# Performance work log

Measured on AMD Instinct MI355X. Metric: run time of the kernel, lower is better.

Reference implementation:

```python
import jax, jax.numpy as jnp
import numpy as np

B, S, D = 4, 2048, 1024
E, K, H = 8, 2, 4096


def setup_inputs() -> dict:
    key = jax.random.key(0)
    ks = jax.random.split(key, 8)
    sd = 1.0 / np.sqrt(D)
    sh = 1.0 / np.sqrt(H)
    x = jax.random.normal(ks[0], (B, S, D), dtype=jnp.float32)
    gate_w = jax.random.normal(ks[1], (D, E), dtype=jnp.float32) * sd
    gate_b = jnp.zeros((E,), dtype=jnp.float32)
    w1 = jax.random.normal(ks[2], (E, D, H), dtype=jnp.float32) * sd
    b1 = jnp.zeros((E, H), dtype=jnp.float32)
    w2 = jax.random.normal(ks[3], (E, H, D), dtype=jnp.float32) * sh
    b2 = jnp.zeros((E, D), dtype=jnp.float32)
    return {"x": x, "gate_w": gate_w, "gate_b": gate_b,
            "w1": w1, "b1": b1, "w2": w2, "b2": b2}


def reference(x, gate_w, gate_b, w1, b1, w2, b2):
    # gate logits [B,S,E]
    logits = jnp.einsum('bsd,de->bse', x, gate_w) + gate_b
    # top-k over experts, softmax over the k selected (dim=2), in float32
    weights, selected = jax.lax.top_k(logits, K)            # [B,S,K]
    weights = jax.nn.softmax(weights.astype(jnp.float32), axis=-1).astype(x.dtype)
    out = jnp.zeros_like(x)
    for i in range(E):
        # per-token combine weight for expert i (0 if not routed here)
        w_i = jnp.sum(jnp.where(selected == i, weights, 0.0), axis=-1)  # [B,S]
        h = jax.nn.gelu(jnp.einsum('bsd,dh->bsh', x, w1[i]) + b1[i])    # [B,S,H]
        y = jnp.einsum('bsh,hd->bsd', h, w2[i]) + b2[i]                  # [B,S,D]
        out = out + w_i[..., None] * y
    return out
```

## Files before the change

kernel.cpp:

```cpp
#include <hip/hip_runtime.h>
#include <hip/hip_bf16.h>
#include <stdint.h>

#define T_TOK 8192
#define D_DIM 1024
#define E_NUM 8
#define H_DIM 4096
#define WL_MAX 72

typedef short bf16x8 __attribute__((ext_vector_type(8)));
typedef float f32x4 __attribute__((ext_vector_type(4)));

#define AS1 __attribute__((address_space(1)))
#define AS3 __attribute__((address_space(3)))

__device__ __forceinline__ unsigned short f2b(float f) {
  union { float f; uint32_t u; } v; v.f = f;
  uint32_t r = (v.u + 0x7fffu + ((v.u >> 16) & 1u)) >> 16;
  return (unsigned short)r;
}

__device__ __forceinline__ float gelu_tanh(float x) {
  float u = 0.7978845608028654f * (x + 0.044715f * x * x * x);
  u = fminf(fmaxf(u, -15.f), 15.f);
  float e = __expf(2.f * u);
  float t = (e - 1.f) / (e + 1.f);
  return 0.5f * x * (1.f + t);
}

__device__ __forceinline__ void gload_lds16(const void* g, void* l) {
  __builtin_amdgcn_global_load_lds((const AS1 uint32_t*)g, (AS3 uint32_t*)l, 16, 0, 0);
}

__global__ __launch_bounds__(256) void moe_gate_conv(const float* __restrict__ x,
                                                     const float* __restrict__ gw,
                                                     const float* __restrict__ gb,
                                                     unsigned short* __restrict__ xb,
                                                     int2* __restrict__ sel,
                                                     float2* __restrict__ wts,
                                                     int* __restrict__ meta) {
  int lane = threadIdx.x & 63;
  int t = blockIdx.x * 4 + (threadIdx.x >> 6);
  const float* xr = x + (size_t)t * D_DIM;
  unsigned short* xo = xb + (size_t)t * D_DIM;
  float acc[8];
#pragma unroll
  for (int e = 0; e < 8; e++) acc[e] = 0.f;
#pragma unroll
  for (int i = 0; i < 4; i++) {
    int d0 = lane * 4 + i * 256;
    float4 xv = *(const float4*)(xr + d0);
    ushort4 o;
    o.x = f2b(xv.x); o.y = f2b(xv.y); o.z = f2b(xv.z); o.w = f2b(xv.w);
    *(ushort4*)(xo + d0) = o;
    const float* gp = gw + (size_t)d0 * 8;
    float xs[4] = {xv.x, xv.y, xv.z, xv.w};
#pragma unroll
    for (int j = 0; j < 4; j++) {
#pragma unroll
      for (int e = 0; e < 8; e++) acc[e] += xs[j] * gp[j * 8 + e];
    }
  }
#pragma unroll
  for (int off = 32; off > 0; off >>= 1) {
#pragma unroll
    for (int e = 0; e < 8; e++) acc[e] += __shfl_xor(acc[e], off);
  }
  if (lane == 0) {
    float lg[8];
#pragma unroll
    for (int e = 0; e < 8; e++) lg[e] = acc[e] + gb[e];
    int e0 = 0; float b0 = lg[0];
#pragma unroll
    for (int e = 1; e < 8; e++) if (lg[e] > b0) { b0 = lg[e]; e0 = e; }
    int e1 = -1; float b1v = -1e30f;
#pragma unroll
    for (int e = 0; e < 8; e++) if (e != e0 && lg[e] > b1v) { b1v = lg[e]; e1 = e; }
    float d = __expf(b1v - b0);
    float w0 = 1.f / (1.f + d), w1 = d / (1.f + d);
    sel[t] = make_int2(e0, e1);
    wts[t] = make_float2(w0, w1);
    atomicAdd(&meta[e0], 1);
    atomicAdd(&meta[e1], 1);
  }
}

__global__ __launch_bounds__(256) void moe_transpose(const float* __restrict__ in,
                                                     unsigned short* __restrict__ out,
                                                     int R, int C) {
  int e = blockIdx.z;
  int c0 = blockIdx.x * 64, r0 = blockIdx.y * 64;
  __shared__ float tile[64][65];
  const float* ine = in + (size_t)e * R * C;
  unsigned short* oute = out + (size_t)e * R * C;
  int tr = threadIdx.x >> 2;
  int tc4 = (threadIdx.x & 3) * 16;
#pragma unroll
  for (int p = 0; p < 4; p++) {
    int c = tc4 + p * 4;
    float4 v = *(const float4*)(ine + (size_t)(r0 + tr) * C + c0 + c);
    tile[tr][c] = v.x; tile[tr][c + 1] = v.y; tile[tr][c + 2] = v.z; tile[tr][c + 3] = v.w;
  }
  __syncthreads();
#pragma unroll
  for (int p = 0; p < 4; p++) {
    int rr = tc4 + p * 4;
    ushort4 o;
    o.x = f2b(tile[rr + 0][tr]);
    o.y = f2b(tile[rr + 1][tr]);
    o.z = f2b(tile[rr + 2][tr]);
    o.w = f2b(tile[rr + 3][tr]);
    *(ushort4*)(oute + (size_t)(c0 + tr) * R + r0 + rr) = o;
  }
}

__global__ void moe_scan(int* meta, int2* wl) {
  if (threadIdx.x == 0 && blockIdx.x == 0) {
    int o = 0;
    for (int e = 0; e < 8; e++) { meta[8 + e] = o; meta[20 + e] = o; o += meta[e]; }
    meta[16] = o;
    int w = 0;
    for (int e = 0; e < 8; e++)
      for (int m0 = 0; m0 < meta[e]; m0 += 256) wl[w++] = make_int2(e, m0);
    meta[17] = w;
  }
}

__global__ __launch_bounds__(256) void moe_scatter(const int2* __restrict__ sel,
                                                   const float2* __restrict__ wts,
                                                   int* __restrict__ meta,
                                                   int* __restrict__ token_id,
                                                   float* __restrict__ weightv) {
  int t = blockIdx.x * 256 + threadIdx.x;
  if (t >= T_TOK) return;
  int2 s = sel[t];
  float2 w = wts[t];
  int p0 = atomicAdd(&meta[20 + s.x], 1); token_id[p0] = t; weightv[p0] = w.x;
  int p1 = atomicAdd(&meta[20 + s.y], 1); token_id[p1] = t; weightv[p1] = w.y;
}

__global__ __launch_bounds__(256) void moe_outinit(const int2* __restrict__ sel,
                                                   const float2* __restrict__ wts,
                                                   const float* __restrict__ b2,
                                                   float* __restrict__ out) {
  int t = blockIdx.x;
  int d = threadIdx.x * 4;
  int2 s = sel[t];
  float2 w = wts[t];
  float4 a = *(const float4*)(b2 + (size_t)s.x * D_DIM + d);
  float4 b = *(const float4*)(b2 + (size_t)s.y * D_DIM + d);
  float4 o;
  o.x = w.x * a.x + w.y * b.x;
  o.y = w.x * a.y + w.y * b.y;
  o.z = w.x * a.z + w.y * b.z;
  o.w = w.x * a.w + w.y * b.w;
  *(float4*)(out + (size_t)t * D_DIM + d) = o;
}

template<int MODE>
__global__ __launch_bounds__(512, 2) void moe_gemm_pipe(
    const unsigned short* __restrict__ Amat,
    const unsigned short* __restrict__ Bmat,
    const float* __restrict__ bias,
    const int* __restrict__ meta,
    const int2* __restrict__ wl,
    const int* __restrict__ token_id,
    const float* __restrict__ weightv,
    unsigned short* __restrict__ hout,
    float* __restrict__ yout) {
  constexpr int KLEN = MODE ? 4096 : 1024;
  constexpr int NK   = MODE ? 64 : 32;

  int wi = blockIdx.y;
  if (wi >= meta[17]) return;
  int e = wl[wi].x, m0 = wl[wi].y;
  int seg = meta[8 + e], ne = meta[9 + e] - seg;
  int n0, kbase;
  if (MODE) { n0 = (int)(blockIdx.x >> 1) * 256; kbase = (int)(blockIdx.x & 1) * 2048; }
  else      { n0 = blockIdx.x * 256; kbase = 0; }

  __shared__ unsigned short As[3][8192];
  __shared__ unsigned short Bs[3][8192];

  int tid = threadIdx.x, lane = tid & 63, w = tid >> 6;
  int wm = w >> 2, wn = w & 3;

  int binv = (lane & 0x38) | ((lane ^ (lane >> 2)) & 6) | ((lane ^ (lane >> 2) ^ (lane >> 4)) & 1);

  const unsigned short* aSrc[2];
  const unsigned short* bSrc[2];
#pragma unroll
  for (int q = 0; q < 2; ++q) {
    int lchunk = ((w * 2 + q) << 6) | binv;
    int row = lchunk >> 2;
    int ko = (lchunk & 3) * 8;
    int gi = m0 + row; if (gi >= ne) gi = m0;
    if (MODE) aSrc[q] = Amat + (size_t)(seg + gi) * KLEN + kbase + ko;
    else      aSrc[q] = Amat + (size_t)token_id[seg + gi] * KLEN + ko;
    bSrc[q] = Bmat + (size_t)e * (4096 * 1024) + (size_t)(n0 + row) * KLEN + kbase + ko;
  }

  auto STAGE = [&](int buf, int kt) {
#pragma unroll
    for (int q = 0; q < 2; ++q) {
      gload_lds16(aSrc[q] + kt * 32, &As[buf][(w * 2 + q) * 512]);
      gload_lds16(bSrc[q] + kt * 32, &Bs[buf][(w * 2 + q) * 512]);
    }
  };

  f32x4 acc[8][4] = {};
  const int aoff = (((wm * 128 + (lane & 15)) * 32 + (lane >> 4) * 8)) ^ ((lane & 7) << 3);
  const int boff = (((wn * 64 + (lane & 15)) * 32 + (lane >> 4) * 8)) ^ ((lane & 7) << 3);

  STAGE(0, 0); STAGE(1, 1);

  int cur = 0, sb = 2;
  for (int t = 0; t < NK; ++t) {
    if (t + 1 < NK) { asm volatile("s_waitcnt vmcnt(4)" ::: "memory"); }
    else            { asm volatile("s_waitcnt vmcnt(0)" ::: "memory"); }
    __builtin_amdgcn_s_barrier();
    if (t + 2 < NK) STAGE(sb, t + 2);
    bf16x8 af[8], bv8[4];
#pragma unroll
    for (int mf = 0; mf < 8; ++mf) af[mf] = *(const bf16x8*)&As[cur][aoff + mf * 512];
#pragma unroll
    for (int nf = 0; nf < 4; ++nf) bv8[nf] = *(const bf16x8*)&Bs[cur][boff + nf * 512];
    __builtin_amdgcn_s_setprio(1);
#pragma unroll
    for (int mf = 0; mf < 8; ++mf)
#pragma unroll
      for (int nf = 0; nf < 4; ++nf)
        acc[mf][nf] = __builtin_amdgcn_mfma_f32_16x16x32_bf16(af[mf], bv8[nf], acc[mf][nf], 0, 0, 0);
    __builtin_amdgcn_s_setprio(0);
    __builtin_amdgcn_sched_barrier(0);
    cur = (cur == 2) ? 0 : cur + 1;
    sb  = (sb  == 2) ? 0 : sb  + 1;
  }

  int rb = wm * 128 + (lane >> 4) * 4;
  int cb = n0 + wn * 64 + (lane & 15);
  if (MODE) {
#pragma unroll
    for (int mf = 0; mf < 8; ++mf) {
#pragma unroll
      for (int j = 0; j < 4; ++j) {
        int gi = m0 + rb + mf * 16 + j;
        if (gi < ne) {
          int p = seg + gi;
          int tok = token_id[p];
          float wt = weightv[p];
          float* orow = yout + (size_t)tok * D_DIM + cb;
#pragma unroll
          for (int nf = 0; nf < 4; ++nf)
            atomicAdd(&orow[nf * 16], wt * acc[mf][nf][j]);
        }
      }
    }
  } else {
    const float* be = bias + (size_t)e * H_DIM + cb;
    float bvv[4];
#pragma unroll
    for (int nf = 0; nf < 4; ++nf) bvv[nf] = be[nf * 16];
#pragma unroll
    for (int mf = 0; mf < 8; ++mf) {
#pragma unroll
      for (int j = 0; j < 4; ++j) {
        int gi = m0 + rb + mf * 16 + j;
        if (gi < ne) {
          unsigned short* hrow = hout + (size_t)(seg + gi) * H_DIM + cb;
#pragma unroll
          for (int nf = 0; nf < 4; ++nf)
            hrow[nf * 16] = f2b(gelu_tanh(acc[mf][nf][j] + bvv[nf]));
        }
      }
    }
  }
}

extern "C" void kernel_launch(void* const* d_in, const int* in_sizes, int n_in,
                              void* d_out, int out_size, void* d_ws, size_t ws_size,
                              hipStream_t stream) {
  const float* x      = (const float*)d_in[0];
  const float* gate_w = (const float*)d_in[1];
  const float* gate_b = (const float*)d_in[2];
  const float* w1     = (const float*)d_in[3];
  const float* b1     = (const float*)d_in[4];
  const float* w2     = (const float*)d_in[5];
  const float* b2     = (const float*)d_in[6];
  float* out = (float*)d_out;

  uint8_t* ws = (uint8_t*)d_ws;
  unsigned short* hbuf = (unsigned short*)(ws);
  unsigned short* xb   = (unsigned short*)(ws + 134217728ull);
  unsigned short* w1t  = (unsigned short*)(ws + 150994944ull);
  unsigned short* w2t  = (unsigned short*)(ws + 218103808ull);
  int*    token_id = (int*)  (ws + 285212672ull);
  float*  weightv  = (float*)(ws + 285278208ull);
  float2* wts      = (float2*)(ws + 285343744ull);
  int2*   sel      = (int2*) (ws + 285409280ull);
  int*    meta     = (int*)  (ws + 285474816ull);
  int2*   wl       = (int2*) (ws + 285475328ull);

  hipMemsetAsync(meta, 0, 512, stream);

  moe_gate_conv<<<dim3(T_TOK / 4), 256, 0, stream>>>(x, gate_w, gate_b, xb, sel, wts, meta);
  moe_transpose<<<dim3(H_DIM / 64, D_DIM / 64, E_NUM), 256, 0, stream>>>(w1, w1t, D_DIM, H_DIM);
  moe_transpose<<<dim3(D_DIM / 64, H_DIM / 64, E_NUM), 256, 0, stream>>>(w2, w2t, H_DIM, D_DIM);
  moe_scan<<<1, 64, 0, stream>>>(meta, wl);
  moe_scatter<<<dim3(T_TOK / 256), 256, 0, stream>>>(sel, wts, meta, token_id, weightv);
  moe_outinit<<<dim3(T_TOK), 256, 0, stream>>>(sel, wts, b2, out);

  moe_gemm_pipe<0><<<dim3(H_DIM / 256, WL_MAX), 512, 0, stream>>>(
      xb, w1t, b1, meta, wl, token_id, weightv, hbuf, nullptr);

  moe_gemm_pipe<1><<<dim3((D_DIM / 256) * 2, WL_MAX), 512, 0, stream>>>(
      hbuf, w2t, nullptr, meta, wl, token_id, weightv, nullptr, out);
}
```

Before: 971.7 us.

## Restructure MoE GEMM to 4-stage pipeline with split A/B staging and expert-interleaved grid

After: 975.0 us. No clear change (+0.3%).

```diff
diff --git a/kernel.cpp b/kernel.cpp
--- a/kernel.cpp
+++ b/kernel.cpp
@@ -6,7 +6,7 @@
 #define D_DIM 1024
 #define E_NUM 8
 #define H_DIM 4096
-#define WL_MAX 72
+#define PPX 10
 
 typedef short bf16x8 __attribute__((ext_vector_type(8)));
 typedef float f32x4 __attribute__((ext_vector_type(4)));
@@ -114,15 +114,11 @@
   }
 }
 
-__global__ void moe_scan(int* meta, int2* wl) {
+__global__ void moe_scan(int* meta) {
   if (threadIdx.x == 0 && blockIdx.x == 0) {
     int o = 0;
     for (int e = 0; e < 8; e++) { meta[8 + e] = o; meta[20 + e] = o; o += meta[e]; }
     meta[16] = o;
-    int w = 0;
-    for (int e = 0; e < 8; e++)
-      for (int m0 = 0; m0 < meta[e]; m0 += 256) wl[w++] = make_int2(e, m0);
-    meta[17] = w;
   }
 }
 
@@ -158,12 +154,11 @@
 }
 
 template<int MODE>
-__global__ __launch_bounds__(512, 2) void moe_gemm_pipe(
+__global__ __launch_bounds__(512, 2) void moe_gemm8p(
     const unsigned short* __restrict__ Amat,
     const unsigned short* __restrict__ Bmat,
     const float* __restrict__ bias,
     const int* __restrict__ meta,
-    const int2* __restrict__ wl,
     const int* __restrict__ token_id,
     const float* __restrict__ weightv,
     unsigned short* __restrict__ hout,
@@ -171,70 +166,99 @@
   constexpr int KLEN = MODE ? 4096 : 1024;
   constexpr int NK   = MODE ? 64 : 32;
 
-  int wi = blockIdx.y;
-  if (wi >= meta[17]) return;
-  int e = wl[wi].x, m0 = wl[wi].y;
+  int b = blockIdx.x;
+  int e = b & 7;
+  int u = b >> 3;
+  int n0, ps, kbase;
+  if (MODE) { n0 = (u & 3) * 256; kbase = ((u >> 2) & 1) * 2048; ps = u >> 3; }
+  else      { n0 = (u & 15) * 256; kbase = 0; ps = u >> 4; }
   int seg = meta[8 + e], ne = meta[9 + e] - seg;
-  int n0, kbase;
-  if (MODE) { n0 = (int)(blockIdx.x >> 1) * 256; kbase = (int)(blockIdx.x & 1) * 2048; }
-  else      { n0 = blockIdx.x * 256; kbase = 0; }
-
-  __shared__ unsigned short As[3][8192];
-  __shared__ unsigned short Bs[3][8192];
+  int m0 = ps * 256;
+  if (m0 >= ne) return;
+
+  __shared__ unsigned short As[4][8192];
+  __shared__ unsigned short Bs[4][8192];
 
   int tid = threadIdx.x, lane = tid & 63, w = tid >> 6;
   int wm = w >> 2, wn = w & 3;
 
-  int binv = (lane & 0x38) | ((lane ^ (lane >> 2)) & 6) | ((lane ^ (lane >> 2) ^ (lane >> 4)) & 1);
-
+  int srow = tid >> 2;
+  int sko  = (tid & 3) * 8;
   const unsigned short* aSrc[2];
   const unsigned short* bSrc[2];
 #pragma unroll
-  for (int q = 0; q < 2; ++q) {
-    int lchunk = ((w * 2 + q) << 6) | binv;
-    int row = lchunk >> 2;
-    int ko = (lchunk & 3) * 8;
-    int gi = m0 + row; if (gi >= ne) gi = m0;
-    if (MODE) aSrc[q] = Amat + (size_t)(seg + gi) * KLEN + kbase + ko;
-    else      aSrc[q] = Amat + (size_t)token_id[seg + gi] * KLEN + ko;
-    bSrc[q] = Bmat + (size_t)e * (4096 * 1024) + (size_t)(n0 + row) * KLEN + kbase + ko;
-  }
-
-  auto STAGE = [&](int buf, int kt) {
-#pragma unroll
-    for (int q = 0; q < 2; ++q) {
-      gload_lds16(aSrc[q] + kt * 32, &As[buf][(w * 2 + q) * 512]);
-      gload_lds16(bSrc[q] + kt * 32, &Bs[buf][(w * 2 + q) * 512]);
-    }
+  for (int h = 0; h < 2; ++h) {
+    int gi = m0 + h * 128 + srow; if (gi >= ne) gi = m0;
+    if (MODE) aSrc[h] = Amat + (size_t)(seg + gi) * KLEN + kbase + sko;
+    else      aSrc[h] = Amat + (size_t)token_id[seg + gi] * KLEN + sko;
+    bSrc[h] = Bmat + (size_t)e * (4096 * 1024)
+                   + (size_t)(n0 + h * 128 + srow) * KLEN + kbase + sko;
+  }
+
+  auto stageA = [&](int buf, int kt) {
+#pragma unroll
+    for (int h = 0; h < 2; ++h)
+      gload_lds16(aSrc[h] + kt * 32, &As[buf][h * 4096 + w * 512]);
   };
+  auto stageB = [&](int buf, int kt) {
+#pragma unroll
+    for (int h = 0; h < 2; ++h)
+      gload_lds16(bSrc[h] + kt * 32, &Bs[buf][h * 4096 + w * 512]);
+  };
 
   f32x4 acc[8][4] = {};
-  const int aoff = (((wm * 128 + (lane & 15)) * 32 + (lane >> 4) * 8)) ^ ((lane & 7) << 3);
-  const int boff = (((wn * 64 + (lane & 15)) * 32 + (lane >> 4) * 8)) ^ ((lane & 7) << 3);
-
-  STAGE(0, 0); STAGE(1, 1);
-
-  int cur = 0, sb = 2;
-  for (int t = 0; t < NK; ++t) {
-    if (t + 1 < NK) { asm volatile("s_waitcnt vmcnt(4)" ::: "memory"); }
-    else            { asm volatile("s_waitcnt vmcnt(0)" ::: "memory"); }
+  const int aoff = (wm * 128 + (lane & 15)) * 32 + (lane >> 4) * 8;
+  const int boff = (wn * 64 + (lane & 15)) * 32 + (lane >> 4) * 8;
+
+  stageA(0, 0); stageB(0, 0);
+  stageA(1, 1); stageB(1, 1);
+  stageA(2, 2); stageB(2, 2);
+  asm volatile("s_waitcnt vmcnt(8)" ::: "memory");
+  __builtin_amdgcn_s_barrier();
+
+  for (int T = 0; T < NK; ++T) {
+    int d = T & 3, s = (T + 3) & 3;
+    bool doStage = (T + 3 < NK);
+
+    if (doStage) stageA(s, T + 3);
+    bf16x8 a0[4], bfr[4];
+#pragma unroll
+    for (int mf = 0; mf < 4; ++mf) a0[mf] = *(const bf16x8*)&As[d][aoff + mf * 512];
+#pragma unroll
+    for (int nf = 0; nf < 4; ++nf) bfr[nf] = *(const bf16x8*)&Bs[d][boff + nf * 512];
     __builtin_amdgcn_s_barrier();
-    if (t + 2 < NK) STAGE(sb, t + 2);
-    bf16x8 af[8], bv8[4];
-#pragma unroll
-    for (int mf = 0; mf < 8; ++mf) af[mf] = *(const bf16x8*)&As[cur][aoff + mf * 512];
-#pragma unroll
-    for (int nf = 0; nf < 4; ++nf) bv8[nf] = *(const bf16x8*)&Bs[cur][boff + nf * 512];
+    asm volatile("s_waitcnt lgkmcnt(0)" ::: "memory");
+    __builtin_amdgcn_sched_barrier(0);
     __builtin_amdgcn_s_setprio(1);
 #pragma unroll
-    for (int mf = 0; mf < 8; ++mf)
+    for (int mf = 0; mf < 4; ++mf)
 #pragma unroll
       for (int nf = 0; nf < 4; ++nf)
-        acc[mf][nf] = __builtin_amdgcn_mfma_f32_16x16x32_bf16(af[mf], bv8[nf], acc[mf][nf], 0, 0, 0);
+        acc[mf][nf] = __builtin_amdgcn_mfma_f32_16x16x32_bf16(a0[mf], bfr[nf], acc[mf][nf], 0, 0, 0);
     __builtin_amdgcn_s_setprio(0);
+    __builtin_amdgcn_s_barrier();
+
+    if (doStage) stageB(s, T + 3);
+    bf16x8 a1[4];
+#pragma unroll
+    for (int mf = 0; mf < 4; ++mf) a1[mf] = *(const bf16x8*)&As[d][aoff + (mf + 4) * 512];
+    __builtin_amdgcn_s_barrier();
+    asm volatile("s_waitcnt lgkmcnt(0)" ::: "memory");
     __builtin_amdgcn_sched_barrier(0);
-    cur = (cur == 2) ? 0 : cur + 1;
-    sb  = (sb  == 2) ? 0 : sb  + 1;
+    __builtin_amdgcn_s_setprio(1);
+#pragma unroll
+    for (int mf = 0; mf < 4; ++mf)
+#pragma unroll
+      for (int nf = 0; nf < 4; ++nf)
+        acc[mf + 4][nf] = __builtin_amdgcn_mfma_f32_16x16x32_bf16(a1[mf], bfr[nf], acc[mf + 4][nf], 0, 0, 0);
+    __builtin_amdgcn_s_setprio(0);
+
+    int rem = NK - 1 - T;
+    if (rem >= 3)      { asm volatile("s_waitcnt vmcnt(8)" ::: "memory"); }
+    else if (rem == 2) { asm volatile("s_waitcnt vmcnt(4)" ::: "memory"); }
+    else if (rem == 1) { asm volatile("s_waitcnt vmcnt(0)" ::: "memory"); }
+    __builtin_amdgcn_sched_barrier(0);
+    __builtin_amdgcn_s_barrier();
   }
 
   int rb = wm * 128 + (lane >> 4) * 4;
@@ -299,20 +323,19 @@
   float2* wts      = (float2*)(ws + 285343744ull);
   int2*   sel      = (int2*) (ws + 285409280ull);
   int*    meta     = (int*)  (ws + 285474816ull);
-  int2*   wl       = (int2*) (ws + 285475328ull);
 
   hipMemsetAsync(meta, 0, 512, stream);
 
   moe_gate_conv<<<dim3(T_TOK / 4), 256, 0, stream>>>(x, gate_w, gate_b, xb, sel, wts, meta);
   moe_transpose<<<dim3(H_DIM / 64, D_DIM / 64, E_NUM), 256, 0, stream>>>(w1, w1t, D_DIM, H_DIM);
   moe_transpose<<<dim3(D_DIM / 64, H_DIM / 64, E_NUM), 256, 0, stream>>>(w2, w2t, H_DIM, D_DIM);
-  moe_scan<<<1, 64, 0, stream>>>(meta, wl);
+  moe_scan<<<1, 64, 0, stream>>>(meta);
   moe_scatter<<<dim3(T_TOK / 256), 256, 0, stream>>>(sel, wts, meta, token_id, weightv);
   moe_outinit<<<dim3(T_TOK), 256, 0, stream>>>(sel, wts, b2, out);
 
-  moe_gemm_pipe<0><<<dim3(H_DIM / 256, WL_MAX), 512, 0, stream>>>(
-      xb, w1t, b1, meta, wl, token_id, weightv, hbuf, nullptr);
-
-  moe_gemm_pipe<1><<<dim3((D_DIM / 256) * 2, WL_MAX), 512, 0, stream>>>(
-      hbuf, w2t, nullptr, meta, wl, token_id, weightv, nullptr, out);
-}
+  moe_gemm8p<0><<<dim3(8 * 16 * PPX), 512, 0, stream>>>(
+      xb, w1t, b1, meta, token_id, weightv, hbuf, nullptr);
+
+  moe_gemm8p<1><<<dim3(8 * 4 * 2 * PPX), 512, 0, stream>>>(
+      hbuf, w2t, nullptr, meta, token_id, weightv, nullptr, out);
+}
```
